# Kernel tuning notes

Hardware: AMD Instinct MI355X
Metric: run time of the kernel (lower is better)

Reference implementation:

```python
import jax, jax.numpy as jnp
import numpy as np
from jax import lax

S, B, I, H = 512, 128, 1024, 1024

def setup_inputs() -> dict:
    key = jax.random.key(0)
    k1, k2, k3 = jax.random.split(key, 3)
    scale = 0.02
    return {
        "x": jax.random.normal(k1, (S, B, I), dtype=jnp.float32),
        "w_ih": jax.random.normal(k2, (4 * H, I), dtype=jnp.float32) * scale,
        "w_hh": jax.random.normal(k3, (4 * H, H), dtype=jnp.float32) * scale,
        "b_ih": jnp.zeros((4 * H,), dtype=jnp.float32),
        "b_hh": jnp.zeros((4 * H,), dtype=jnp.float32),
    }

def reference(x, w_ih, w_hh, b_ih, b_hh):
    seq, bsz, _ = x.shape
    hid = w_hh.shape[1]
    # Batch the input-side GEMM across all timesteps at once: [S,B,4H]
    gates_x = jnp.einsum('sbi,gi->sbg', x, w_ih) + b_ih + b_hh

    def step(carry, gx):
        h, c = carry
        gates = gx + h @ w_hh.T                      # [B,4H]
        i, f, g, o = jnp.split(gates, 4, axis=-1)
        i = jax.nn.sigmoid(i)
        f = jax.nn.sigmoid(f)
        g = jnp.tanh(g)
        o = jax.nn.sigmoid(o)
        c = f * c + i * g
        h = o * jnp.tanh(c)
        return (h, c), h

    h0 = jnp.zeros((bsz, hid), dtype=x.dtype)
    c0 = jnp.zeros((bsz, hid), dtype=x.dtype)
    (hN, cN), output = lax.scan(step, (h0, c0), gates_x)
    # output: [S,B,H]; final hidden state (hN, cN) as in the torch module
    return output, hN, cN
```

## Files before the change

### kernel.cpp

```cpp
#include <hip/hip_runtime.h>


#define S_LEN 512

using short8 = __attribute__((ext_vector_type(8))) short;
using f32x4  = __attribute__((ext_vector_type(4))) float;

__device__ __forceinline__ unsigned short f2bf(float f) {
  unsigned int u = __float_as_uint(f);
  u += 0x7fffu + ((u >> 16) & 1u);
  return (unsigned short)(u >> 16);
}
__device__ __forceinline__ unsigned int pk2(float a, float b) {
  return (unsigned int)f2bf(a) | ((unsigned int)f2bf(b) << 16);
}
__device__ __forceinline__ float sigf(float x)  { return 1.f / (1.f + __expf(-x)); }
__device__ __forceinline__ float tanhf_(float x){ return 2.f / (1.f + __expf(-2.f * x)) - 1.f; }

__global__ void xpack_kernel(const float* __restrict__ x, unsigned short* __restrict__ xp) {
  const int gid = blockIdx.x * 256 + threadIdx.x;
  const int t  = gid >> 14;
  const int u  = gid & 16383;
  const int ln = u & 63;
  const int u6 = u >> 6;
  const int rf = u6 & 3;
  const int ks = (u6 >> 2) & 7;
  const int kq = (u6 >> 5) & 3;
  const int rh = u6 >> 7;
  const int row = rh * 64 + rf * 16 + (ln & 15);
  const int i   = kq * 256 + ks * 32 + (ln >> 4) * 8;
  const float* src = x + ((size_t)t * 131072 + (size_t)row * 1024 + i);
  const float4 v0 = *(const float4*)src;
  const float4 v1 = *(const float4*)(src + 4);
  uint4 o;
  o.x = pk2(v0.x, v0.y); o.y = pk2(v0.z, v0.w);
  o.z = pk2(v1.x, v1.y); o.w = pk2(v1.z, v1.w);
  *(uint4*)(xp + (size_t)gid * 8) = o;
}

__global__ void wpack_kernel(const float* __restrict__ w_hh, const float* __restrict__ w_ih,
                             unsigned short* __restrict__ wp) {
  const int gid = blockIdx.x * 256 + threadIdx.x;
  const int ln = gid & 63;
  const int u6 = gid >> 6;
  const int cg = u6 & 3;
  const int ks = (u6 >> 2) & 7;
  const int kq = (u6 >> 5) & 7;
  const int b  = u6 >> 8;
  const int grow = cg * 1024 + b * 16 + (ln & 15);
  const int k    = kq * 256 + ks * 32 + (ln >> 4) * 8;
  const float* src = (k < 1024) ? (w_hh + (size_t)grow * 1024 + k)
                                : (w_ih + (size_t)grow * 1024 + (k - 1024));
  const float4 v0 = *(const float4*)src;
  const float4 v1 = *(const float4*)(src + 4);
  uint4 o;
  o.x = pk2(v0.x, v0.y); o.y = pk2(v0.z, v0.w);
  o.z = pk2(v1.x, v1.y); o.w = pk2(v1.z, v1.w);
  *(uint4*)(wp + (size_t)gid * 8) = o;
}

__global__ void bias_sum_kernel(const float* __restrict__ a, const float* __restrict__ b,
                                float* __restrict__ o, int n) {
  int i = blockIdx.x * blockDim.x + threadIdx.x;
  if (i < n) o[i] = a[i] + b[i];
}

__global__ __launch_bounds__(512) void lstm_step(
    const unsigned short* __restrict__ hp_in,
    const unsigned short* __restrict__ xp_t,
    const unsigned short* __restrict__ wp,
    const float* __restrict__ bias,
    float* __restrict__ cbuf,
    float* __restrict__ out_t,
    unsigned short* __restrict__ hp_out)
{
  __shared__ f32x4 P[8][2][4][64];
  __shared__ f32x4 G[2][4][64];
  const int tid  = threadIdx.x;
  const int lane = tid & 63;
  const int w    = tid >> 6;
  const int rq   = blockIdx.x >> 6;
  const int b    = blockIdx.x & 63;
  const int rh   = rq >> 1;
  const int rfb  = (rq & 1) * 2;

  const unsigned short* ab = ((w < 4) ? hp_in : xp_t) + (size_t)(rh * 4 + (w & 3)) * 16384;
  const unsigned short* bb = wp + (size_t)(b * 8 + w) * 16384;

  const int fr = tid >> 8;
  const int qc = (tid >> 6) & 3;
  const int rc = (tid >> 4) & 3;
  const int hc = tid & 15;
  const int j   = b * 16 + hc;
  const int row = rq * 32 + fr * 16 + qc * 4 + rc;
  const size_t idx = (size_t)row * 1024 + j;
  const float b0 = bias[j];
  const float b1 = bias[1024 + j];
  const float b2 = bias[2048 + j];
  const float b3 = bias[3072 + j];
  const float cold = cbuf[idx];

  short8 afr[3][2], bfr[3][4];
#pragma unroll
  for (int p = 0; p < 2; ++p) {
#pragma unroll
    for (int f = 0; f < 2; ++f) afr[p][f] = *(const short8*)(ab + (p * 4 + rfb + f) * 512 + lane * 8);
#pragma unroll
    for (int cg = 0; cg < 4; ++cg) bfr[p][cg] = *(const short8*)(bb + (p * 4 + cg) * 512 + lane * 8);
  }

  f32x4 acc[2][4] = {};
#pragma unroll
  for (int ks = 0; ks < 8; ++ks) {
    const int cur = ks % 3;
    if (ks < 6) {
      const int nxt = (ks + 2) % 3;
#pragma unroll
      for (int f = 0; f < 2; ++f)
        afr[nxt][f] = *(const short8*)(ab + ((ks + 2) * 4 + rfb + f) * 512 + lane * 8);
#pragma unroll
      for (int cg = 0; cg < 4; ++cg)
        bfr[nxt][cg] = *(const short8*)(bb + ((ks + 2) * 4 + cg) * 512 + lane * 8);
    }
#pragma unroll
    for (int f = 0; f < 2; ++f)
#pragma unroll
      for (int cg = 0; cg < 4; ++cg)
        acc[f][cg] = __builtin_amdgcn_mfma_f32_16x16x32_bf16(afr[cur][f], bfr[cur][cg], acc[f][cg], 0, 0, 0);
  }

#pragma unroll
  for (int f = 0; f < 2; ++f)
#pragma unroll
    for (int cg = 0; cg < 4; ++cg)
      P[w][f][cg][lane] = acc[f][cg];
  __syncthreads();
  {
    const int rf_e = w >> 2;
    const int cg_e = w & 3;
    f32x4 s = P[0][rf_e][cg_e][lane];
#pragma unroll
    for (int kq = 1; kq < 8; ++kq) s += P[kq][rf_e][cg_e][lane];
    G[rf_e][cg_e][lane] = s;
  }
  __syncthreads();

  const float* Gp = (const float*)G;
  const int gbase = (fr * 4) * 256 + (qc * 16 + hc) * 4 + rc;
  const float g0 = Gp[gbase];
  const float g1 = Gp[gbase + 256];
  const float g2 = Gp[gbase + 512];
  const float g3 = Gp[gbase + 768];

  const float iv = sigf(g0 + b0);
  const float fv = sigf(g1 + b1);
  const float gv = tanhf_(g2 + b2);
  const float ov = sigf(g3 + b3);
  const float cc = fv * cold + iv * gv;
  cbuf[idx] = cc;
  const float hh = ov * tanhf_(cc);
  out_t[idx] = hh;
  const int kqm = j >> 8, ksj = (j >> 5) & 7, qj = (j >> 3) & 3, ej = j & 7;
  const int rhj = row >> 6, rfj = (row >> 4) & 3, rj = row & 15;
  hp_out[(size_t)((((rhj * 4 + kqm) * 8 + ksj) * 4 + rfj) * 64 + (qj * 16 + rj)) * 8 + ej] = f2bf(hh);
}

extern "C" void kernel_launch(void* const* d_in, const int* in_sizes, int n_in,
                              void* d_out, int out_size, void* d_ws, size_t ws_size,
                              hipStream_t stream) {
  (void)in_sizes; (void)n_in; (void)out_size; (void)ws_size;
  const float* x    = (const float*)d_in[0];
  const float* w_ih = (const float*)d_in[1];
  const float* w_hh = (const float*)d_in[2];
  const float* b_ih = (const float*)d_in[3];
  const float* b_hh = (const float*)d_in[4];
  float* out = (float*)d_out;

  char* ws = (char*)d_ws;
  const size_t XP_OFF   = 0;
  const size_t WP_OFF   = XP_OFF + 134217728;
  const size_t BIAS_OFF = WP_OFF + 16777216;
  const size_t C_OFF    = BIAS_OFF + 16384;
  const size_t H0_OFF   = C_OFF + 524288;
  const size_t H1_OFF   = H0_OFF + 262144;

  unsigned short* xp   = (unsigned short*)(ws + XP_OFF);
  unsigned short* wp   = (unsigned short*)(ws + WP_OFF);
  float*          bias = (float*)(ws + BIAS_OFF);
  float*          cbuf = (float*)(ws + C_OFF);
  unsigned short* h0   = (unsigned short*)(ws + H0_OFF);
  unsigned short* h1   = (unsigned short*)(ws + H1_OFF);

  xpack_kernel<<<32768, 256, 0, stream>>>(x, xp);
  wpack_kernel<<<4096, 256, 0, stream>>>(w_hh, w_ih, wp);
  bias_sum_kernel<<<16, 256, 0, stream>>>(b_ih, b_hh, bias, 4096);
  hipMemsetAsync(cbuf, 0, 524288, stream);
  hipMemsetAsync(h0, 0, 262144, stream);

  unsigned short* hin = h0;
  unsigned short* hout = h1;
  for (int t = 0; t < S_LEN; ++t) {
    lstm_step<<<256, 512, 0, stream>>>(hin, xp + (size_t)t * 131072, wp, bias, cbuf,
                                       out + (size_t)t * 131072, hout);
    unsigned short* tmp = hin; hin = hout; hout = tmp;
  }

  hipMemcpyAsync(out + (size_t)S_LEN * 131072, out + (size_t)(S_LEN - 1) * 131072,
                 131072 * sizeof(float), hipMemcpyDeviceToDevice, stream);
  hipMemcpyAsync(out + (size_t)S_LEN * 131072 + 131072, cbuf,
                 131072 * sizeof(float), hipMemcpyDeviceToDevice, stream);
}
```

Baseline: 4.978 ms.

## Replace per-timestep launches with a persistent cooperative LSTM kernel

The 512 per-step kernel launches are replaced by one cooperative kernel that loops over timesteps and uses grid.sync between steps. Weight fragments are loaded into registers once and reused across all steps, and the cell state stays in a register instead of round-tripping through global memory. The final h and c copies are folded into the last iteration. The aim is to remove launch overhead and repeated weight and cell-state traffic. The cost is higher register pressure from 32 short8 weight fragments per thread, and the need for all 256 blocks to be co-resident at once.

New measurement: 17.71 ms. 256% more time.

```diff
diff --git a/kernel.cpp b/kernel.cpp
--- a/kernel.cpp
+++ b/kernel.cpp
@@ -1,4 +1,7 @@
 #include <hip/hip_runtime.h>
+#include <hip/hip_cooperative_groups.h>
+
+namespace cg = cooperative_groups;
 
 
 #define S_LEN 512
@@ -65,14 +68,13 @@
   if (i < n) o[i] = a[i] + b[i];
 }
 
-__global__ __launch_bounds__(512) void lstm_step(
-    const unsigned short* __restrict__ hp_in,
-    const unsigned short* __restrict__ xp_t,
+__global__ __launch_bounds__(512, 2) void lstm_persist(
+    const unsigned short* __restrict__ xp,
     const unsigned short* __restrict__ wp,
     const float* __restrict__ bias,
-    float* __restrict__ cbuf,
-    float* __restrict__ out_t,
-    unsigned short* __restrict__ hp_out)
+    unsigned short* __restrict__ h0,
+    unsigned short* __restrict__ h1,
+    float* __restrict__ out)
 {
   __shared__ f32x4 P[8][2][4][64];
   __shared__ f32x4 G[2][4][64];
@@ -83,9 +85,15 @@
   const int b    = blockIdx.x & 63;
   const int rh   = rq >> 1;
   const int rfb  = (rq & 1) * 2;
-
-  const unsigned short* ab = ((w < 4) ? hp_in : xp_t) + (size_t)(rh * 4 + (w & 3)) * 16384;
+  const size_t aoff = (size_t)(rh * 4 + (w & 3)) * 16384;
+
   const unsigned short* bb = wp + (size_t)(b * 8 + w) * 16384;
+  short8 wreg[8][4];
+#pragma unroll
+  for (int ks = 0; ks < 8; ++ks)
+#pragma unroll
+    for (int cg = 0; cg < 4; ++cg)
+      wreg[ks][cg] = *(const short8*)(bb + (ks * 4 + cg) * 512 + lane * 8);
 
   const int fr = tid >> 8;
   const int qc = (tid >> 6) & 3;
@@ -98,71 +106,80 @@
   const float b1 = bias[1024 + j];
   const float b2 = bias[2048 + j];
   const float b3 = bias[3072 + j];
-  const float cold = cbuf[idx];
-
-  short8 afr[3][2], bfr[3][4];
-#pragma unroll
-  for (int p = 0; p < 2; ++p) {
-#pragma unroll
-    for (int f = 0; f < 2; ++f) afr[p][f] = *(const short8*)(ab + (p * 4 + rfb + f) * 512 + lane * 8);
-#pragma unroll
-    for (int cg = 0; cg < 4; ++cg) bfr[p][cg] = *(const short8*)(bb + (p * 4 + cg) * 512 + lane * 8);
-  }
-
-  f32x4 acc[2][4] = {};
-#pragma unroll
-  for (int ks = 0; ks < 8; ++ks) {
-    const int cur = ks % 3;
-    if (ks < 6) {
-      const int nxt = (ks + 2) % 3;
-#pragma unroll
-      for (int f = 0; f < 2; ++f)
-        afr[nxt][f] = *(const short8*)(ab + ((ks + 2) * 4 + rfb + f) * 512 + lane * 8);
-#pragma unroll
-      for (int cg = 0; cg < 4; ++cg)
-        bfr[nxt][cg] = *(const short8*)(bb + ((ks + 2) * 4 + cg) * 512 + lane * 8);
-    }
-#pragma unroll
-    for (int f = 0; f < 2; ++f)
-#pragma unroll
-      for (int cg = 0; cg < 4; ++cg)
-        acc[f][cg] = __builtin_amdgcn_mfma_f32_16x16x32_bf16(afr[cur][f], bfr[cur][cg], acc[f][cg], 0, 0, 0);
-  }
-
-#pragma unroll
-  for (int f = 0; f < 2; ++f)
-#pragma unroll
-    for (int cg = 0; cg < 4; ++cg)
-      P[w][f][cg][lane] = acc[f][cg];
-  __syncthreads();
-  {
-    const int rf_e = w >> 2;
-    const int cg_e = w & 3;
-    f32x4 s = P[0][rf_e][cg_e][lane];
-#pragma unroll
-    for (int kq = 1; kq < 8; ++kq) s += P[kq][rf_e][cg_e][lane];
-    G[rf_e][cg_e][lane] = s;
-  }
-  __syncthreads();
-
-  const float* Gp = (const float*)G;
-  const int gbase = (fr * 4) * 256 + (qc * 16 + hc) * 4 + rc;
-  const float g0 = Gp[gbase];
-  const float g1 = Gp[gbase + 256];
-  const float g2 = Gp[gbase + 512];
-  const float g3 = Gp[gbase + 768];
-
-  const float iv = sigf(g0 + b0);
-  const float fv = sigf(g1 + b1);
-  const float gv = tanhf_(g2 + b2);
-  const float ov = sigf(g3 + b3);
-  const float cc = fv * cold + iv * gv;
-  cbuf[idx] = cc;
-  const float hh = ov * tanhf_(cc);
-  out_t[idx] = hh;
+  float creg = 0.f;
   const int kqm = j >> 8, ksj = (j >> 5) & 7, qj = (j >> 3) & 3, ej = j & 7;
   const int rhj = row >> 6, rfj = (row >> 4) & 3, rj = row & 15;
-  hp_out[(size_t)((((rhj * 4 + kqm) * 8 + ksj) * 4 + rfj) * 64 + (qj * 16 + rj)) * 8 + ej] = f2bf(hh);
+  const size_t hpk = (size_t)((((rhj * 4 + kqm) * 8 + ksj) * 4 + rfj) * 64 + (qj * 16 + rj)) * 8 + ej;
+  const int gbase = (fr * 4) * 256 + (qc * 16 + hc) * 4 + rc;
+
+  cg::grid_group grid = cg::this_grid();
+
+  for (int t = 0; t < S_LEN; ++t) {
+    const unsigned short* hin = (t & 1) ? h1 : h0;
+    unsigned short*       hout = (t & 1) ? h0 : h1;
+    const unsigned short* ab = ((w < 4) ? hin : (xp + (size_t)t * 131072)) + aoff;
+
+    short8 afr[3][2];
+#pragma unroll
+    for (int p = 0; p < 2; ++p)
+#pragma unroll
+      for (int f = 0; f < 2; ++f)
+        afr[p][f] = *(const short8*)(ab + (p * 4 + rfb + f) * 512 + lane * 8);
+
+    f32x4 acc[2][4] = {};
+#pragma unroll
+    for (int ks = 0; ks < 8; ++ks) {
+      const int cur = ks % 3;
+      if (ks < 6) {
+        const int nxt = (ks + 2) % 3;
+#pragma unroll
+        for (int f = 0; f < 2; ++f)
+          afr[nxt][f] = *(const short8*)(ab + ((ks + 2) * 4 + rfb + f) * 512 + lane * 8);
+      }
+#pragma unroll
+      for (int f = 0; f < 2; ++f)
+#pragma unroll
+        for (int cg = 0; cg < 4; ++cg)
+          acc[f][cg] = __builtin_amdgcn_mfma_f32_16x16x32_bf16(afr[cur][f], wreg[ks][cg], acc[f][cg], 0, 0, 0);
+    }
+
+#pragma unroll
+    for (int f = 0; f < 2; ++f)
+#pragma unroll
+      for (int cg = 0; cg < 4; ++cg)
+        P[w][f][cg][lane] = acc[f][cg];
+    __syncthreads();
+    {
+      const int rf_e = w >> 2;
+      const int cg_e = w & 3;
+      f32x4 s = P[0][rf_e][cg_e][lane];
+#pragma unroll
+      for (int kq = 1; kq < 8; ++kq) s += P[kq][rf_e][cg_e][lane];
+      G[rf_e][cg_e][lane] = s;
+    }
+    __syncthreads();
+
+    const float* Gp = (const float*)G;
+    const float g0 = Gp[gbase];
+    const float g1 = Gp[gbase + 256];
+    const float g2 = Gp[gbase + 512];
+    const float g3 = Gp[gbase + 768];
+
+    const float iv = sigf(g0 + b0);
+    const float fv = sigf(g1 + b1);
+    const float gv = tanhf_(g2 + b2);
+    const float ov = sigf(g3 + b3);
+    creg = fv * creg + iv * gv;
+    const float hh = ov * tanhf_(creg);
+    out[(size_t)t * 131072 + idx] = hh;
+    hout[hpk] = f2bf(hh);
+    if (t == S_LEN - 1) {
+      out[(size_t)S_LEN * 131072 + idx] = hh;
+      out[(size_t)S_LEN * 131072 + 131072 + idx] = creg;
+    }
+
+    if (t < S_LEN - 1) grid.sync();
+  }
 }
 
 extern "C" void kernel_launch(void* const* d_in, const int* in_sizes, int n_in,
@@ -180,33 +197,21 @@
   const size_t XP_OFF   = 0;
   const size_t WP_OFF   = XP_OFF + 134217728;
   const size_t BIAS_OFF = WP_OFF + 16777216;
-  const size_t C_OFF    = BIAS_OFF + 16384;
-  const size_t H0_OFF   = C_OFF + 524288;
+  const size_t H0_OFF   = BIAS_OFF + 16384;
   const size_t H1_OFF   = H0_OFF + 262144;
 
   unsigned short* xp   = (unsigned short*)(ws + XP_OFF);
   unsigned short* wp   = (unsigned short*)(ws + WP_OFF);
   float*          bias = (float*)(ws + BIAS_OFF);
-  float*          cbuf = (float*)(ws + C_OFF);
   unsigned short* h0   = (unsigned short*)(ws + H0_OFF);
   unsigned short* h1   = (unsigned short*)(ws + H1_OFF);
 
   xpack_kernel<<<32768, 256, 0, stream>>>(x, xp);
   wpack_kernel<<<4096, 256, 0, stream>>>(w_hh, w_ih, wp);
   bias_sum_kernel<<<16, 256, 0, stream>>>(b_ih, b_hh, bias, 4096);
-  hipMemsetAsync(cbuf, 0, 524288, stream);
   hipMemsetAsync(h0, 0, 262144, stream);
 
-  unsigned short* hin = h0;
-  unsigned short* hout = h1;
-  for (int t = 0; t < S_LEN; ++t) {
-    lstm_step<<<256, 512, 0, stream>>>(hin, xp + (size_t)t * 131072, wp, bias, cbuf,
-                                       out + (size_t)t * 131072, hout);
-    unsigned short* tmp = hin; hin = hout; hout = tmp;
-  }
-
-  hipMemcpyAsync(out + (size_t)S_LEN * 131072, out + (size_t)(S_LEN - 1) * 131072,
-                 131072 * sizeof(float), hipMemcpyDeviceToDevice, stream);
-  hipMemcpyAsync(out + (size_t)S_LEN * 131072 + 131072, cbuf,
-                 131072 * sizeof(float), hipMemcpyDeviceToDevice, stream);
-}
+  void* args[] = {(void*)&xp, (void*)&wp, (void*)&bias, (void*)&h0, (void*)&h1, (void*)&out};
+  hipLaunchCooperativeKernel((const void*)lstm_persist, dim3(256), dim3(512),
+                             args, 0, stream);
+}
```

## Hoist input GEMM out of recurrence into chunked batched pre-GEMM

Applied to the files above, without the earlier changes.

The input-side projection x·W_ih is moved out of each per-step kernel into a batched pre-GEMM, computed per 32-timestep chunk with W_ih tiles staged in LDS. The recurrent step kernel now only multiplies h by W_hh and adds precomputed fp32 gate inputs that already include the bias. This halves the per-step MFMA work and weight traffic on the serial critical path. The cost is extra fp32 gate-buffer traffic and one pack plus one pre-GEMM launch per chunk, which run serialized on the stream.

New measurement: 4.114 ms. 17.3% less time.

```diff
diff --git a/kernel.cpp b/kernel.cpp
--- a/kernel.cpp
+++ b/kernel.cpp
@@ -2,6 +2,8 @@
 
 
 #define S_LEN 512
+#define CS 32
+#define NCHUNK (S_LEN / CS)
 
 using short8 = __attribute__((ext_vector_type(8))) short;
 using f32x4  = __attribute__((ext_vector_type(4))) float;
@@ -17,46 +19,43 @@
 __device__ __forceinline__ float sigf(float x)  { return 1.f / (1.f + __expf(-x)); }
 __device__ __forceinline__ float tanhf_(float x){ return 2.f / (1.f + __expf(-2.f * x)) - 1.f; }
 
-__global__ void xpack_kernel(const float* __restrict__ x, unsigned short* __restrict__ xp) {
+__global__ void xpack_chunk(const float* __restrict__ x, unsigned short* __restrict__ xpc,
+                            int t0) {
   const int gid = blockIdx.x * 256 + threadIdx.x;
-  const int t  = gid >> 14;
+  const int tc = gid >> 14;
   const int u  = gid & 16383;
   const int ln = u & 63;
   const int u6 = u >> 6;
   const int rf = u6 & 3;
-  const int ks = (u6 >> 2) & 7;
-  const int kq = (u6 >> 5) & 3;
+  const int kk = (u6 >> 2) & 31;
   const int rh = u6 >> 7;
   const int row = rh * 64 + rf * 16 + (ln & 15);
-  const int i   = kq * 256 + ks * 32 + (ln >> 4) * 8;
-  const float* src = x + ((size_t)t * 131072 + (size_t)row * 1024 + i);
+  const int i   = kk * 32 + (ln >> 4) * 8;
+  const float* src = x + ((size_t)(t0 + tc) * 131072 + (size_t)row * 1024 + i);
   const float4 v0 = *(const float4*)src;
   const float4 v1 = *(const float4*)(src + 4);
   uint4 o;
   o.x = pk2(v0.x, v0.y); o.y = pk2(v0.z, v0.w);
   o.z = pk2(v1.x, v1.y); o.w = pk2(v1.z, v1.w);
-  *(uint4*)(xp + (size_t)gid * 8) = o;
-}
-
-__global__ void wpack_kernel(const float* __restrict__ w_hh, const float* __restrict__ w_ih,
-                             unsigned short* __restrict__ wp) {
+  *(uint4*)(xpc + (size_t)gid * 8) = o;
+}
+
+__global__ void wpack_kernel(const float* __restrict__ w, unsigned short* __restrict__ wpk) {
   const int gid = blockIdx.x * 256 + threadIdx.x;
   const int ln = gid & 63;
   const int u6 = gid >> 6;
   const int cg = u6 & 3;
-  const int ks = (u6 >> 2) & 7;
-  const int kq = (u6 >> 5) & 7;
-  const int b  = u6 >> 8;
+  const int kk = (u6 >> 2) & 31;
+  const int b  = u6 >> 7;
   const int grow = cg * 1024 + b * 16 + (ln & 15);
-  const int k    = kq * 256 + ks * 32 + (ln >> 4) * 8;
-  const float* src = (k < 1024) ? (w_hh + (size_t)grow * 1024 + k)
-                                : (w_ih + (size_t)grow * 1024 + (k - 1024));
+  const int k    = kk * 32 + (ln >> 4) * 8;
+  const float* src = w + (size_t)grow * 1024 + k;
   const float4 v0 = *(const float4*)src;
   const float4 v1 = *(const float4*)(src + 4);
   uint4 o;
   o.x = pk2(v0.x, v0.y); o.y = pk2(v0.z, v0.w);
   o.z = pk2(v1.x, v1.y); o.w = pk2(v1.z, v1.w);
-  *(uint4*)(wp + (size_t)gid * 8) = o;
+  *(uint4*)(wpk + (size_t)gid * 8) = o;
 }
 
 __global__ void bias_sum_kernel(const float* __restrict__ a, const float* __restrict__ b,
@@ -65,11 +64,61 @@
   if (i < n) o[i] = a[i] + b[i];
 }
 
-__global__ __launch_bounds__(512) void lstm_step(
+__global__ __launch_bounds__(512, 2) void pregemm_kernel(
+    const unsigned short* __restrict__ xpc,
+    const unsigned short* __restrict__ wi,
+    const float* __restrict__ bias,
+    float* __restrict__ gxc)
+{
+  __shared__ short Bs[65536];
+  const int tid  = threadIdx.x;
+  const int lane = tid & 63;
+  const int w    = tid >> 6;
+  const int tc   = blockIdx.x >> 6;
+  const int b    = blockIdx.x & 63;
+
+  {
+    const unsigned short* wb = wi + (size_t)b * 65536;
+#pragma unroll
+    for (int i = 0; i < 16; ++i) {
+      const int fi = w * 16 + i;
+      *(short8*)&Bs[fi * 512 + lane * 8] = *(const short8*)(wb + (size_t)fi * 512 + lane * 8);
+    }
+  }
+  __syncthreads();
+
+  const int rh = w >> 2, rf = w & 3;
+  const unsigned short* ab = xpc + (size_t)tc * 131072 + (size_t)(rh * 32 * 4 + rf) * 512;
+
+  f32x4 acc[4] = {};
+#pragma unroll
+  for (int kk = 0; kk < 32; ++kk) {
+    const short8 a = *(const short8*)(ab + (size_t)kk * 2048 + lane * 8);
+#pragma unroll
+    for (int cg = 0; cg < 4; ++cg) {
+      const short8 bf = *(const short8*)&Bs[(kk * 4 + cg) * 512 + lane * 8];
+      acc[cg] = __builtin_amdgcn_mfma_f32_16x16x32_bf16(a, bf, acc[cg], 0, 0, 0);
+    }
+  }
+
+  const int q   = lane >> 4;
+  const int c15 = lane & 15;
+  const int j   = b * 16 + c15;
+#pragma unroll
+  for (int cg = 0; cg < 4; ++cg) {
+    const float bv = bias[cg * 1024 + j];
+#pragma unroll
+    for (int r = 0; r < 4; ++r) {
+      const int row = w * 16 + q * 4 + r;
+      gxc[(size_t)((tc * 4 + cg) * 128 + row) * 1024 + j] = acc[cg][r] + bv;
+    }
+  }
+}
+
+__global__ __launch_bounds__(512, 2) void lstm_step(
     const unsigned short* __restrict__ hp_in,
-    const unsigned short* __restrict__ xp_t,
-    const unsigned short* __restrict__ wp,
-    const float* __restrict__ bias,
+    const float* __restrict__ gx_t,
+    const unsigned short* __restrict__ wh,
     float* __restrict__ cbuf,
     float* __restrict__ out_t,
     unsigned short* __restrict__ hp_out)
@@ -84,9 +133,6 @@
   const int rh   = rq >> 1;
   const int rfb  = (rq & 1) * 2;
 
-  const unsigned short* ab = ((w < 4) ? hp_in : xp_t) + (size_t)(rh * 4 + (w & 3)) * 16384;
-  const unsigned short* bb = wp + (size_t)(b * 8 + w) * 16384;
-
   const int fr = tid >> 8;
   const int qc = (tid >> 6) & 3;
   const int rc = (tid >> 4) & 3;
@@ -94,40 +140,34 @@
   const int j   = b * 16 + hc;
   const int row = rq * 32 + fr * 16 + qc * 4 + rc;
   const size_t idx = (size_t)row * 1024 + j;
-  const float b0 = bias[j];
-  const float b1 = bias[1024 + j];
-  const float b2 = bias[2048 + j];
-  const float b3 = bias[3072 + j];
+  const float gx0 = gx_t[(size_t)(0 * 128 + row) * 1024 + j];
+  const float gx1 = gx_t[(size_t)(1 * 128 + row) * 1024 + j];
+  const float gx2 = gx_t[(size_t)(2 * 128 + row) * 1024 + j];
+  const float gx3 = gx_t[(size_t)(3 * 128 + row) * 1024 + j];
   const float cold = cbuf[idx];
 
-  short8 afr[3][2], bfr[3][4];
-#pragma unroll
-  for (int p = 0; p < 2; ++p) {
-#pragma unroll
-    for (int f = 0; f < 2; ++f) afr[p][f] = *(const short8*)(ab + (p * 4 + rfb + f) * 512 + lane * 8);
-#pragma unroll
-    for (int cg = 0; cg < 4; ++cg) bfr[p][cg] = *(const short8*)(bb + (p * 4 + cg) * 512 + lane * 8);
+  const unsigned short* ab = hp_in + (size_t)(rh * 32 + w * 4) * 2048;
+  const unsigned short* bb = wh + (size_t)(b * 32 + w * 4) * 2048;
+
+  short8 afr[4][2], bfr[4][4];
+#pragma unroll
+  for (int s = 0; s < 4; ++s) {
+#pragma unroll
+    for (int f = 0; f < 2; ++f)
+      afr[s][f] = *(const short8*)(ab + (size_t)(s * 4 + rfb + f) * 512 + lane * 8);
+#pragma unroll
+    for (int cg = 0; cg < 4; ++cg)
+      bfr[s][cg] = *(const short8*)(bb + (size_t)(s * 4 + cg) * 512 + lane * 8);
   }
 
   f32x4 acc[2][4] = {};
 #pragma unroll
-  for (int ks = 0; ks < 8; ++ks) {
-    const int cur = ks % 3;
-    if (ks < 6) {
-      const int nxt = (ks + 2) % 3;
-#pragma unroll
-      for (int f = 0; f < 2; ++f)
-        afr[nxt][f] = *(const short8*)(ab + ((ks + 2) * 4 + rfb + f) * 512 + lane * 8);
+  for (int s = 0; s < 4; ++s)
+#pragma unroll
+    for (int f = 0; f < 2; ++f)
 #pragma unroll
       for (int cg = 0; cg < 4; ++cg)
-        bfr[nxt][cg] = *(const short8*)(bb + ((ks + 2) * 4 + cg) * 512 + lane * 8);
-    }
-#pragma unroll
-    for (int f = 0; f < 2; ++f)
-#pragma unroll
-      for (int cg = 0; cg < 4; ++cg)
-        acc[f][cg] = __builtin_amdgcn_mfma_f32_16x16x32_bf16(afr[cur][f], bfr[cur][cg], acc[f][cg], 0, 0, 0);
-  }
+        acc[f][cg] = __builtin_amdgcn_mfma_f32_16x16x32_bf16(afr[s][f], bfr[s][cg], acc[f][cg], 0, 0, 0);
 
 #pragma unroll
   for (int f = 0; f < 2; ++f)
@@ -147,22 +187,17 @@
 
   const float* Gp = (const float*)G;
   const int gbase = (fr * 4) * 256 + (qc * 16 + hc) * 4 + rc;
-  const float g0 = Gp[gbase];
-  const float g1 = Gp[gbase + 256];
-  const float g2 = Gp[gbase + 512];
-  const float g3 = Gp[gbase + 768];
-
-  const float iv = sigf(g0 + b0);
-  const float fv = sigf(g1 + b1);
-  const float gv = tanhf_(g2 + b2);
-  const float ov = sigf(g3 + b3);
+  const float iv = sigf(Gp[gbase]       + gx0);
+  const float fv = sigf(Gp[gbase + 256] + gx1);
+  const float gv = tanhf_(Gp[gbase + 512] + gx2);
+  const float ov = sigf(Gp[gbase + 768] + gx3);
   const float cc = fv * cold + iv * gv;
   cbuf[idx] = cc;
   const float hh = ov * tanhf_(cc);
   out_t[idx] = hh;
-  const int kqm = j >> 8, ksj = (j >> 5) & 7, qj = (j >> 3) & 3, ej = j & 7;
+  const int kkj = j >> 5, qj = (j >> 3) & 3, ej = j & 7;
   const int rhj = row >> 6, rfj = (row >> 4) & 3, rj = row & 15;
-  hp_out[(size_t)((((rhj * 4 + kqm) * 8 + ksj) * 4 + rfj) * 64 + (qj * 16 + rj)) * 8 + ej] = f2bf(hh);
+  hp_out[(size_t)(((rhj * 32 + kkj) * 4 + rfj) * 64 + (qj * 16 + rj)) * 8 + ej] = f2bf(hh);
 }
 
 extern "C" void kernel_launch(void* const* d_in, const int* in_sizes, int n_in,
@@ -177,32 +212,42 @@
   float* out = (float*)d_out;
 
   char* ws = (char*)d_ws;
-  const size_t XP_OFF   = 0;
-  const size_t WP_OFF   = XP_OFF + 134217728;
-  const size_t BIAS_OFF = WP_OFF + 16777216;
+  const size_t XPC_OFF  = 0;
+  const size_t GXC_OFF  = XPC_OFF + 8388608;
+  const size_t WH_OFF   = GXC_OFF + 67108864;
+  const size_t WI_OFF   = WH_OFF + 8388608;
+  const size_t BIAS_OFF = WI_OFF + 8388608;
   const size_t C_OFF    = BIAS_OFF + 16384;
   const size_t H0_OFF   = C_OFF + 524288;
   const size_t H1_OFF   = H0_OFF + 262144;
 
-  unsigned short* xp   = (unsigned short*)(ws + XP_OFF);
-  unsigned short* wp   = (unsigned short*)(ws + WP_OFF);
+  unsigned short* xpc  = (unsigned short*)(ws + XPC_OFF);
+  float*          gxc  = (float*)(ws + GXC_OFF);
+  unsigned short* wh   = (unsigned short*)(ws + WH_OFF);
+  unsigned short* wi   = (unsigned short*)(ws + WI_OFF);
   float*          bias = (float*)(ws + BIAS_OFF);
   float*          cbuf = (float*)(ws + C_OFF);
   unsigned short* h0   = (unsigned short*)(ws + H0_OFF);
   unsigned short* h1   = (unsigned short*)(ws + H1_OFF);
 
-  xpack_kernel<<<32768, 256, 0, stream>>>(x, xp);
-  wpack_kernel<<<4096, 256, 0, stream>>>(w_hh, w_ih, wp);
+  wpack_kernel<<<2048, 256, 0, stream>>>(w_hh, wh);
+  wpack_kernel<<<2048, 256, 0, stream>>>(w_ih, wi);
   bias_sum_kernel<<<16, 256, 0, stream>>>(b_ih, b_hh, bias, 4096);
   hipMemsetAsync(cbuf, 0, 524288, stream);
   hipMemsetAsync(h0, 0, 262144, stream);
 
   unsigned short* hin = h0;
   unsigned short* hout = h1;
-  for (int t = 0; t < S_LEN; ++t) {
-    lstm_step<<<256, 512, 0, stream>>>(hin, xp + (size_t)t * 131072, wp, bias, cbuf,
-                                       out + (size_t)t * 131072, hout);
-    unsigned short* tmp = hin; hin = hout; hout = tmp;
+  for (int c = 0; c < NCHUNK; ++c) {
+    const int t0 = c * CS;
+    xpack_chunk<<<2048, 256, 0, stream>>>(x, xpc, t0);
+    pregemm_kernel<<<2048, 512, 0, stream>>>(xpc, wi, bias, gxc);
+    for (int s = 0; s < CS; ++s) {
+      const int t = t0 + s;
+      lstm_step<<<256, 512, 0, stream>>>(hin, gxc + (size_t)s * 524288, wh, cbuf,
+                                         out + (size_t)t * 131072, hout);
+      unsigned short* tmp = hin; hin = hout; hout = tmp;
+    }
   }
 
   hipMemcpyAsync(out + (size_t)S_LEN * 131072, out + (size_t)(S_LEN - 1) * 131072,
```
